# Kernel tuning notes

Hardware: AMD Instinct MI355X
Metric: run time of the kernel (lower is better)

## Reference

```python
import jax, jax.numpy as jnp
import numpy as np

N_NODES = 100000
N_EDGES = 1000000
N_RELS = 8
N_HEADS = 4
IN_FEAT = 64
OUT_FEAT = 64
D_HEAD = OUT_FEAT // N_HEADS
LEAKY_SLOPE = 0.2


def setup_inputs() -> dict:
    key = jax.random.key(0)
    ks = jax.random.split(key, 8)
    x = jax.random.normal(ks[0], (N_NODES, IN_FEAT), dtype=jnp.float32)
    src_idx = jax.random.randint(ks[1], (N_EDGES,), 0, N_NODES)
    dst_idx = jax.random.randint(ks[2], (N_EDGES,), 0, N_NODES)
    edge_rel = jnp.sort(jax.random.randint(ks[3], (N_EDGES,), 0, N_RELS))
    # xavier-ish small init for weights
    conv_weights = jax.random.normal(ks[4], (N_RELS, N_HEADS, IN_FEAT, D_HEAD), dtype=jnp.float32) * 0.1
    attn_l = jax.random.normal(ks[5], (N_RELS, N_HEADS, D_HEAD), dtype=jnp.float32) * 0.1
    attn_r = jax.random.normal(ks[6], (N_RELS, N_HEADS, D_HEAD), dtype=jnp.float32) * 0.1
    h_bias = jnp.zeros((OUT_FEAT,), dtype=jnp.float32)
    return {
        'x': x, 'src_idx': src_idx, 'dst_idx': dst_idx, 'edge_rel': edge_rel,
        'conv_weights': conv_weights, 'attn_l': attn_l, 'attn_r': attn_r,
        'h_bias': h_bias,
    }


def reference(x, src_idx, dst_idx, edge_rel, conv_weights, attn_l, attn_r, h_bias):
    N = x.shape[0]
    # Per-relation transform of all node features: [R, N, H, D]
    feat_all = jnp.einsum('ni,rhid->rnhd', x, conv_weights)
    # Per-relation attention logits per node: [R, N, H]
    el_all = jnp.einsum('rnhd,rhd->rnh', feat_all, attn_l)
    er_all = jnp.einsum('rnhd,rhd->rnh', feat_all, attn_r)
    # Gather per-edge quantities (relation-specific transform of src/dst)
    feat_e = feat_all[edge_rel, src_idx]          # [E, H, D]
    el = el_all[edge_rel, src_idx]                # [E, H]
    er = er_all[edge_rel, dst_idx]                # [E, H]
    s = jax.nn.leaky_relu(el + er, negative_slope=LEAKY_SLOPE)
    # Edge softmax over incoming edges of each destination node (per head)
    m = jax.ops.segment_max(s, dst_idx, num_segments=N)      # [N, H]
    e = jnp.exp(s - m[dst_idx])                               # [E, H]
    denom = jax.ops.segment_sum(e, dst_idx, num_segments=N)   # [N, H]
    w = e / jnp.maximum(denom[dst_idx], jnp.float32(1e-16))   # [E, H]
    # Weighted aggregation of source features into destination nodes
    agg = jax.ops.segment_sum(feat_e * w[..., None], dst_idx, num_segments=N)  # [N, H, D]
    h = agg.reshape(N, OUT_FEAT) + h_bias
    # activation=None, dropout in eval mode -> identity
    return h
```

## Files before the change

### kernel.cpp

```cpp
#include <hip/hip_runtime.h>
#include <hip/hip_bf16.h>

#define NN 100000
#define NE 1000000
#define NR 8

#define EB 1024
#define NBLK 977
#define NBUCK 196
#define NT (NBUCK*NBLK)
#define NBB 749

#define K3DPB 32
#define K3CAP 160

#define K0_BLKS  160
#define PRE_BLKS (K0_BLKS + NBLK)

typedef unsigned short u16;
typedef unsigned int u32;
typedef __attribute__((ext_vector_type(8))) short bf16x8;
typedef __attribute__((ext_vector_type(4))) float f32x4;

static __device__ __forceinline__ float bf2f(u16 u) {
    union { u32 i; float f; } v; v.i = ((u32)u) << 16; return v.f;
}
static __device__ __forceinline__ float bflo(u32 u) {
    union { u32 i; float f; } v; v.i = u << 16; return v.f;
}
static __device__ __forceinline__ float bfhi(u32 u) {
    union { u32 i; float f; } v; v.i = u & 0xffff0000u; return v.f;
}
static __device__ __forceinline__ u16 f2bf(float f) {
    __hip_bfloat16 h = __float2bfloat16(f);
    return *reinterpret_cast<u16*>(&h);
}
static __device__ __forceinline__ float ldf(const void* p, int idx, int isf32) {
    return isf32 ? ((const float*)p)[idx] : bf2f(((const u16*)p)[idx]);
}

static __device__ __forceinline__ int detect_wave(const u16* xw, int lane)
{
    int insane = 0;
    for (int k = lane; k < 512; k += 64) {
        u16 w = xw[k];
        int ex = (w >> 7) & 0xFF;
        bool sane = ((w & 0x7FFF) == 0) || (ex >= 96 && ex <= 159);
        insane += sane ? 0 : 1;
    }
    for (int off = 32; off; off >>= 1) insane += __shfl_down(insane, off);
    return insane;
}

__global__ __launch_bounds__(256) void k_pre(
    const void* __restrict__ xin, int* __restrict__ flag,
    const void* __restrict__ cw, const void* __restrict__ al,
    const void* __restrict__ ar, u16* __restrict__ Bpre,
    const int* __restrict__ dsti, int* __restrict__ histT)
{
    __shared__ int sflag;
    __shared__ int hist[NBUCK];
    int t = threadIdx.x;
    int b = blockIdx.x;

    if (b < K0_BLKS) {
        if (t < 64) {
            int insane = detect_wave((const u16*)xin, t);
            if (t == 0) {
                sflag = (insane > 50) ? 1 : 0;
                if (b == 0) *flag = sflag;
            }
        }
        __syncthreads();
        int isf32 = sflag;
        int tid = b * 256 + t;
        if (tid >= NR * 5120) return;
        int r = tid / 5120, rem = tid % 5120;
        int c = rem >> 3, j = rem & 7;
        int nt = c >> 7, kk = (c >> 6) & 1, lc = c & 63;
        int i = kk * 32 + ((lc >> 4) << 3) + j;
        int d = lc & 15;
        u16 val;
        if (nt < 4) {
            val = f2bf(ldf(cw, ((r * 4 + nt) * 64 + i) * 16 + d, isf32));
        } else if (d < 8) {
            int h = d >> 1;
            const void* attn = (d & 1) ? ar : al;
            float s = 0.f;
            for (int dd = 0; dd < 16; ++dd)
                s += ldf(cw, ((r * 4 + h) * 64 + i) * 16 + dd, isf32)
                   * ldf(attn, (r * 4 + h) * 16 + dd, isf32);
            val = f2bf(s);
        } else {
            val = 0;
        }
        Bpre[tid] = val;
    } else {
        int blk = b - K0_BLKS;
        if (t < NBUCK) hist[t] = 0;
        __syncthreads();
        int base = blk * EB;
        for (int j = 0; j < EB; j += 256) {
            int e = base + j + t;
            if (e < NE) atomicAdd(&hist[dsti[e] >> 9], 1);
        }
        __syncthreads();
        if (t < NBUCK) histT[t * NBLK + blk] = hist[t];
    }
}

__global__ __launch_bounds__(256) void k1_feat(
    const void* __restrict__ xin, const u16* __restrict__ Bpre,
    u16* __restrict__ feat_all, float* __restrict__ el_all, float* __restrict__ er_all)
{
    __shared__ u32 ldsT[2][64][32];
    int n0 = blockIdx.x * 64;
    int tid = threadIdx.x;
    int wave = tid >> 6, lane = tid & 63;
    int col = lane & 15, quad = lane >> 4;

    int insane = detect_wave((const u16*)xin, lane);
    insane = __shfl(insane, 0);
    int isf32 = (insane > 50) ? 1 : 0;

    int node = n0 + wave * 16 + col;
    int nclamp = node < NN ? node : NN - 1;
    bool nvalid = node < NN;

    bf16x8 afrag0, afrag1;
    if (!isf32) {
        const u16* xb = (const u16*)xin + nclamp * 64 + quad * 8;
        afrag0 = *(const bf16x8*)&xb[0];
        afrag1 = *(const bf16x8*)&xb[32];
    } else {
        const float* xf = (const float*)xin + nclamp * 64 + quad * 8;
#pragma unroll
        for (int j = 0; j < 8; ++j) {
            afrag0[j] = (short)f2bf(xf[j]);
            afrag1[j] = (short)f2bf(xf[32 + j]);
        }
    }

#pragma unroll 1
    for (int ch = 0; ch < 4; ++ch) {
#pragma unroll
        for (int rr = 0; rr < 2; ++rr) {
            int r = ch * 2 + rr;
            f32x4 acc[5];
#pragma unroll
            for (int nt = 0; nt < 5; ++nt) acc[nt] = f32x4{0.f, 0.f, 0.f, 0.f};
#pragma unroll
            for (int nt = 0; nt < 5; ++nt) {
                bf16x8 b0 = *(const bf16x8*)&Bpre[r * 5120 + ((nt * 2 + 0) * 64 + lane) * 8];
                bf16x8 b1 = *(const bf16x8*)&Bpre[r * 5120 + ((nt * 2 + 1) * 64 + lane) * 8];
                acc[nt] = __builtin_amdgcn_mfma_f32_16x16x32_bf16(b0, afrag0, acc[nt], 0, 0, 0);
                acc[nt] = __builtin_amdgcn_mfma_f32_16x16x32_bf16(b1, afrag1, acc[nt], 0, 0, 0);
            }

#pragma unroll
            for (int nt = 0; nt < 4; ++nt) {
                u32 lo = (u32)f2bf(acc[nt][0]) | ((u32)f2bf(acc[nt][1]) << 16);
                u32 hi = (u32)f2bf(acc[nt][2]) | ((u32)f2bf(acc[nt][3]) << 16);
                int w = (nt * 8 + quad * 2) ^ (col * 2);
                *(uint2*)&ldsT[rr][wave * 16 + col][w] = uint2{lo, hi};
            }
            if (nvalid && quad < 2) {
                int eb = (r * NN + node) * 4 + quad * 2;
                *(float2*)&el_all[eb] = float2{acc[4][0], acc[4][2]};
                *(float2*)&er_all[eb] = float2{acc[4][1], acc[4][3]};
            }
        }
        __syncthreads();

#pragma unroll
        for (int it = 0; it < 8; ++it) {
            int u = it * 256 + tid;
            int rr = u >> 10;
            int v = u & 1023;
            int nl = v >> 4;
            int p  = v & 15;
            int w  = (p * 2) ^ ((nl & 15) * 2);
            uint2 val = *(const uint2*)&ldsT[rr][nl][w];
            int nd = n0 + nl;
            if (nd < NN)
                *(uint2*)&feat_all[((ch * 2 + rr) * NN + nd) * 64 + p * 4] = val;
        }
        __syncthreads();
    }
}

__global__ __launch_bounds__(256) void k_scanB1(int* __restrict__ histT,
                                                int* __restrict__ bsum)
{
    __shared__ int wtot[4];
    int t = threadIdx.x;
    int gi = blockIdx.x * 256 + t;
    int v = (gi < NT) ? histT[gi] : 0;
    int lane = t & 63, w = t >> 6;
    int s = v;
#pragma unroll
    for (int m = 1; m < 64; m <<= 1) {
        int u = __shfl_up(s, m);
        if (lane >= m) s += u;
    }
    if (lane == 63) wtot[w] = s;
    __syncthreads();
    int wb = 0;
    for (int i = 0; i < w; ++i) wb += wtot[i];
    if (gi < NT) histT[gi] = wb + s - v;
    if (t == 255) bsum[blockIdx.x] = wb + s;
}

__global__ __launch_bounds__(1024) void k_scanB2(const int* __restrict__ bsum,
                                                 int* __restrict__ boff,
                                                 const int* __restrict__ histT,
                                                 int* __restrict__ bstart)
{
    __shared__ int wtot[16];
    __shared__ int sboff[NBB];
    int t = threadIdx.x;
    int v = (t < NBB) ? bsum[t] : 0;
    int lane = t & 63, w = t >> 6;
    int s = v;
#pragma unroll
    for (int m = 1; m < 64; m <<= 1) {
        int u = __shfl_up(s, m);
        if (lane >= m) s += u;
    }
    if (lane == 63) wtot[w] = s;
    __syncthreads();
    int wb = 0;
    for (int i = 0; i < w; ++i) wb += wtot[i];
    if (t < NBB) {
        int val = wb + s - v;
        boff[t] = val;
        sboff[t] = val;
    }
    __syncthreads();
    if (t < NBUCK) {
        int gi = t * NBLK;
        bstart[t] = histT[gi] + sboff[gi >> 8];
    }
    if (t == 0) bstart[NBUCK] = NE;
}

__global__ __launch_bounds__(256) void k_binC(
    const int* __restrict__ srci, const int* __restrict__ dsti,
    const int* __restrict__ reli, const int* __restrict__ histT,
    const int* __restrict__ boff, int* __restrict__ key_b)
{
    __shared__ int cur[NBUCK];
    int t = threadIdx.x, blk = blockIdx.x;
    if (t < NBUCK) {
        int gi = t * NBLK + blk;
        cur[t] = histT[gi] + boff[gi >> 8];
    }
    __syncthreads();
    int base = blk * EB;
    for (int j = 0; j < EB; j += 256) {
        int e = base + j + t;
        if (e < NE) {
            int d = dsti[e];
            int key = ((d & 511) << 20) | (reli[e] << 17) | srci[e];
            int pos = atomicAdd(&cur[d >> 9], 1);
            key_b[pos] = key;
        }
    }
}

__global__ __launch_bounds__(1024) void k_binD(
    const int* __restrict__ bstart, const int* __restrict__ key_b,
    int* __restrict__ key_s, int* __restrict__ off)
{
    __shared__ int cnt[512];
    __shared__ int wtot[8];
    int t = threadIdx.x, b = blockIdx.x;
    int s0 = bstart[b], s1 = bstart[b + 1];
    if (t < 512) cnt[t] = 0;
    __syncthreads();
    for (int j = s0 + t; j < s1; j += 1024)
        atomicAdd(&cnt[(key_b[j] >> 20) & 511], 1);
    __syncthreads();
    int excl = 0;
    if (t < 512) {
        int v = cnt[t];
        int lane = t & 63, w = t >> 6;
        int s = v;
#pragma unroll
        for (int m = 1; m < 64; m <<= 1) {
            int u = __shfl_up(s, m);
            if (lane >= m) s += u;
        }
        if (lane == 63) wtot[w] = s;
        __syncthreads();
        int wb = 0;
        for (int i = 0; i < w; ++i) wb += wtot[i];
        excl = s0 + wb + s - v;
        int d = (b << 9) + t;
        if (d < NN) off[d] = excl;
    } else {
        __syncthreads();
    }
    __syncthreads();
    if (t < 512) cnt[t] = excl;
    if (b == 0 && t == 0) off[NN] = NE;
    __syncthreads();
    for (int j = s0 + t; j < s1; j += 1024) {
        int key = key_b[j];
        int pos = atomicAdd(&cnt[(key >> 20) & 511], 1);
        key_s[pos] = key;
    }
}

__global__ __launch_bounds__(256) void k3_node(
    const int* __restrict__ off, const int* __restrict__ key_s,
    const float* __restrict__ el_all, const float* __restrict__ er_all,
    const u16* __restrict__ feat_all, const void* __restrict__ bias,
    const int* __restrict__ flag, void* __restrict__ out)
{
    __shared__ int   ldsOffs[K3DPB + 1];
    __shared__ int   ldsKey[4][K3CAP];
    __shared__ float ldsEE[4][K3CAP][4];
    int t = threadIdx.x;
    int wave = t >> 6, lane = t & 63;
    int dg = lane >> 3;
    int fl = lane & 7;
    int h  = fl >> 1;
    int d0 = blockIdx.x * K3DPB;
    int isf32 = *flag;

    if (t < K3DPB + 1) ldsOffs[t] = off[min(d0 + t, NN)];
    __syncthreads();

    int dlo = wave * 8;
    int estart = ldsOffs[dlo], eend = ldsOffs[dlo + 8];
    int scount = min(eend - estart, K3CAP);

    int dbase = d0 & ~511;
    for (int j = lane; j < scount; j += 64) {
        int key = key_s[estart + j];
        int rel = (key >> 17) & 7, src = key & 131071;
        int d = dbase | ((key >> 20) & 511);
        int kk = rel * NN + src;
        f32x4 el = *(const f32x4*)&el_all[kk * 4];
        f32x4 er = *(const f32x4*)&er_all[(rel * NN + d) * 4];
        f32x4 ee;
#pragma unroll
        for (int q = 0; q < 4; ++q) {
            float v = el[q] + er[q];
            v = v > 0.f ? v : 0.2f * v;
            ee[q] = __expf(v);
        }
        ldsKey[wave][j] = kk;
        *(f32x4*)&ldsEE[wave][j][0] = ee;
    }

    float bv[8];
#pragma unroll
    for (int q = 0; q < 8; ++q) bv[q] = ldf(bias, fl * 8 + q, isf32);

    int nl = dlo + dg;
    int d = d0 + nl;
    int s  = ldsOffs[nl] - estart;
    int e1 = ldsOffs[nl + 1] - estart;
    float acc[8] = {0.f, 0.f, 0.f, 0.f, 0.f, 0.f, 0.f, 0.f};
    float accW = 0.f;

    int e1c = min(e1, K3CAP);
    for (int base = s; base < e1c; base += 4) {
        int kk[4]; float w[4];
#pragma unroll
        for (int q = 0; q < 4; ++q) {
            int idx = base + q;
            bool vld = idx < e1c;
            kk[q] = vld ? ldsKey[wave][idx] : ldsKey[wave][base];
            w[q]  = vld ? ldsEE[wave][idx][h] : 0.f;
        }
        uint4 u[4];
#pragma unroll
        for (int q = 0; q < 4; ++q)
            u[q] = *(const uint4*)&feat_all[kk[q] * 64 + fl * 8];
#pragma unroll
        for (int q = 0; q < 4; ++q) {
            acc[0] += bflo(u[q].x) * w[q];
            acc[1] += bfhi(u[q].x) * w[q];
            acc[2] += bflo(u[q].y) * w[q];
            acc[3] += bfhi(u[q].y) * w[q];
            acc[4] += bflo(u[q].z) * w[q];
            acc[5] += bfhi(u[q].z) * w[q];
            acc[6] += bflo(u[q].w) * w[q];
            acc[7] += bfhi(u[q].w) * w[q];
            accW += w[q];
        }
    }
    for (int j = max(s, K3CAP); j < e1; ++j) {
        int key = key_s[estart + j];
        int rel = (key >> 17) & 7, src = key & 131071;
        int kk0 = rel * NN + src;
        float v = el_all[kk0 * 4 + h] + er_all[(rel * NN + d) * 4 + h];
        v = v > 0.f ? v : 0.2f * v;
        float w0 = __expf(v);
        uint4 u = *(const uint4*)&feat_all[kk0 * 64 + fl * 8];
        acc[0] += bflo(u.x) * w0;
        acc[1] += bfhi(u.x) * w0;
        acc[2] += bflo(u.y) * w0;
        acc[3] += bfhi(u.y) * w0;
        acc[4] += bflo(u.z) * w0;
        acc[5] += bfhi(u.z) * w0;
        acc[6] += bflo(u.w) * w0;
        acc[7] += bfhi(u.w) * w0;
        accW += w0;
    }

    {
        float invh = 1.f / fmaxf(accW, 1e-16f);
        float o[8];
#pragma unroll
        for (int q = 0; q < 8; ++q) o[q] = acc[q] * invh + bv[q];
        if (isf32) {
            ((f32x4*)out)[d * 16 + fl * 2]     = f32x4{o[0], o[1], o[2], o[3]};
            ((f32x4*)out)[d * 16 + fl * 2 + 1] = f32x4{o[4], o[5], o[6], o[7]};
        } else {
            uint4 st;
            st.x = (u32)f2bf(o[0]) | ((u32)f2bf(o[1]) << 16);
            st.y = (u32)f2bf(o[2]) | ((u32)f2bf(o[3]) << 16);
            st.z = (u32)f2bf(o[4]) | ((u32)f2bf(o[5]) << 16);
            st.w = (u32)f2bf(o[6]) | ((u32)f2bf(o[7]) << 16);
            *(uint4*)&((u16*)out)[d * 64 + fl * 8] = st;
        }
    }
}

extern "C" void kernel_launch(void* const* d_in, const int* in_sizes, int n_in,
                              void* d_out, int out_size, void* d_ws, size_t ws_size,
                              hipStream_t stream)
{
    const void* x   = d_in[0];
    const int* srci = (const int*)d_in[1];
    const int* dsti = (const int*)d_in[2];
    const int* reli = (const int*)d_in[3];
    const void* cw  = d_in[4];
    const void* al  = d_in[5];
    const void* ar  = d_in[6];
    const void* hb  = d_in[7];

    char* ws = (char*)d_ws;
    u16*   feat_all = (u16*)  (ws + 0);
    float* el_all   = (float*)(ws + 102400000);
    float* er_all   = (float*)(ws + 115200000);
    int*   key_s    = (int*)  (ws + 128000000);
    int*   key_b    = (int*)  (ws + 132000000);
    int*   off      = (int*)  (ws + 136000000);
    int*   histT    = (int*)  (ws + 136400064);
    int*   bsum     = (int*)  (ws + 137166032);
    int*   boff     = (int*)  (ws + 137169040);
    int*   bstart   = (int*)  (ws + 137172048);
    u16*   Bpre     = (u16*)  (ws + 137172880);
    int*   flag     = (int*)  (ws + 137254800);

    k_pre<<<PRE_BLKS, 256, 0, stream>>>(x, flag, cw, al, ar, Bpre, dsti, histT);
    k1_feat<<<(NN + 63) / 64, 256, 0, stream>>>(x, Bpre, feat_all, el_all, er_all);
    k_scanB1<<<NBB, 256, 0, stream>>>(histT, bsum);
    k_scanB2<<<1, 1024, 0, stream>>>(bsum, boff, histT, bstart);
    k_binC<<<NBLK, 256, 0, stream>>>(srci, dsti, reli, histT, boff, key_b);
    k_binD<<<NBUCK, 1024, 0, stream>>>(bstart, key_b, key_s, off);
    k3_node<<<(NN + 31) / 32, 256, 0, stream>>>(off, key_s, el_all, er_all, feat_all,
                                                hb, flag, d_out);
}
```

Baseline: 201.6 us.

## Interleave feature transform blocks with sort stages in fused launches

Splits the dense per-relation feature transform (k1) into four chunks and co-launches each chunk alongside one stage of the destination-sort pipeline (scan1, scan2, binning, per-bucket sort) in a single fused kernel with a shared LDS buffer. The latency-bound sort stages, especially the single-block scan, now run concurrently with compute-heavy MFMA blocks instead of serially. scanB2 and binD are rewritten to use 256 threads with carried multi-pass scans, so the fused kernel has a uniform block size. The tradeoff is a larger shared-memory footprint for every block, which can lower occupancy, plus more branching and uneven work across blocks.

```diff
diff --git a/kernel.cpp b/kernel.cpp
--- a/kernel.cpp
+++ b/kernel.cpp
@@ -16,6 +16,12 @@
 
 #define K0_BLKS  160
 #define PRE_BLKS (K0_BLKS + NBLK)
+
+#define K1CH 1563
+#define F1K 390
+#define F2K 390
+#define F3K 391
+#define F4K 392
 
 typedef unsigned short u16;
 typedef unsigned int u32;
@@ -109,12 +115,13 @@
     }
 }
 
-__global__ __launch_bounds__(256) void k1_feat(
+static __device__ __forceinline__ void k1_body(
+    int cb, unsigned char* smem,
     const void* __restrict__ xin, const u16* __restrict__ Bpre,
     u16* __restrict__ feat_all, float* __restrict__ el_all, float* __restrict__ er_all)
 {
-    __shared__ u32 ldsT[2][64][32];
-    int n0 = blockIdx.x * 64;
+    u32 (*ldsT)[64][32] = (u32 (*)[64][32])smem;
+    int n0 = cb * 64;
     int tid = threadIdx.x;
     int wave = tid >> 6, lane = tid & 63;
     int col = lane & 15, quad = lane >> 4;
@@ -156,7 +163,6 @@
                 acc[nt] = __builtin_amdgcn_mfma_f32_16x16x32_bf16(b0, afrag0, acc[nt], 0, 0, 0);
                 acc[nt] = __builtin_amdgcn_mfma_f32_16x16x32_bf16(b1, afrag1, acc[nt], 0, 0, 0);
             }
-
 #pragma unroll
             for (int nt = 0; nt < 4; ++nt) {
                 u32 lo = (u32)f2bf(acc[nt][0]) | ((u32)f2bf(acc[nt][1]) << 16);
@@ -171,7 +177,6 @@
             }
         }
         __syncthreads();
-
 #pragma unroll
         for (int it = 0; it < 8; ++it) {
             int u = it * 256 + tid;
@@ -189,12 +194,12 @@
     }
 }
 
-__global__ __launch_bounds__(256) void k_scanB1(int* __restrict__ histT,
-                                                int* __restrict__ bsum)
-{
-    __shared__ int wtot[4];
+static __device__ __forceinline__ void scanB1_body(
+    int b, unsigned char* smem, int* __restrict__ histT, int* __restrict__ bsum)
+{
+    int* wtot = (int*)smem;
     int t = threadIdx.x;
-    int gi = blockIdx.x * 256 + t;
+    int gi = b * 256 + t;
     int v = (gi < NT) ? histT[gi] : 0;
     int lane = t & 63, w = t >> 6;
     int s = v;
@@ -208,35 +213,40 @@
     int wb = 0;
     for (int i = 0; i < w; ++i) wb += wtot[i];
     if (gi < NT) histT[gi] = wb + s - v;
-    if (t == 255) bsum[blockIdx.x] = wb + s;
-}
-
-__global__ __launch_bounds__(1024) void k_scanB2(const int* __restrict__ bsum,
-                                                 int* __restrict__ boff,
-                                                 const int* __restrict__ histT,
-                                                 int* __restrict__ bstart)
-{
-    __shared__ int wtot[16];
-    __shared__ int sboff[NBB];
+    if (t == 255) bsum[b] = wb + s;
+}
+
+static __device__ __forceinline__ void scanB2_body(
+    unsigned char* smem, const int* __restrict__ bsum, int* __restrict__ boff,
+    const int* __restrict__ histT, int* __restrict__ bstart)
+{
+    int* wtot  = (int*)smem;
+    int* sboff = (int*)(smem + 16);
+    int* carry = (int*)(smem + 16 + 4 * NBB);
     int t = threadIdx.x;
-    int v = (t < NBB) ? bsum[t] : 0;
-    int lane = t & 63, w = t >> 6;
-    int s = v;
-#pragma unroll
-    for (int m = 1; m < 64; m <<= 1) {
-        int u = __shfl_up(s, m);
-        if (lane >= m) s += u;
-    }
-    if (lane == 63) wtot[w] = s;
-    __syncthreads();
-    int wb = 0;
-    for (int i = 0; i < w; ++i) wb += wtot[i];
-    if (t < NBB) {
-        int val = wb + s - v;
-        boff[t] = val;
-        sboff[t] = val;
-    }
-    __syncthreads();
+    if (t == 0) *carry = 0;
+    __syncthreads();
+    for (int c = 0; c < 3; ++c) {
+        int idx = c * 256 + t;
+        int v = (idx < NBB) ? bsum[idx] : 0;
+        int lane = t & 63, w = t >> 6;
+        int s = v;
+#pragma unroll
+        for (int m = 1; m < 64; m <<= 1) {
+            int u = __shfl_up(s, m);
+            if (lane >= m) s += u;
+        }
+        if (lane == 63) wtot[w] = s;
+        __syncthreads();
+        int wb = 0;
+        for (int i = 0; i < w; ++i) wb += wtot[i];
+        int ex = *carry + wb + s - v;
+        if (idx < NBB) sboff[idx] = ex;
+        __syncthreads();
+        if (t == 255) *carry += wb + s;
+        __syncthreads();
+    }
+    for (int i = t; i < NBB; i += 256) boff[i] = sboff[i];
     if (t < NBUCK) {
         int gi = t * NBLK;
         bstart[t] = histT[gi] + sboff[gi >> 8];
@@ -244,19 +254,20 @@
     if (t == 0) bstart[NBUCK] = NE;
 }
 
-__global__ __launch_bounds__(256) void k_binC(
+static __device__ __forceinline__ void binC_body(
+    int b, unsigned char* smem,
     const int* __restrict__ srci, const int* __restrict__ dsti,
     const int* __restrict__ reli, const int* __restrict__ histT,
     const int* __restrict__ boff, int* __restrict__ key_b)
 {
-    __shared__ int cur[NBUCK];
-    int t = threadIdx.x, blk = blockIdx.x;
+    int* cur = (int*)smem;
+    int t = threadIdx.x;
     if (t < NBUCK) {
-        int gi = t * NBLK + blk;
+        int gi = t * NBLK + b;
         cur[t] = histT[gi] + boff[gi >> 8];
     }
     __syncthreads();
-    int base = blk * EB;
+    int base = b * EB;
     for (int j = 0; j < EB; j += 256) {
         int e = base + j + t;
         if (e < NE) {
@@ -268,22 +279,26 @@
     }
 }
 
-__global__ __launch_bounds__(1024) void k_binD(
+static __device__ __forceinline__ void binD_body(
+    int b, unsigned char* smem,
     const int* __restrict__ bstart, const int* __restrict__ key_b,
     int* __restrict__ key_s, int* __restrict__ off)
 {
-    __shared__ int cnt[512];
-    __shared__ int wtot[8];
-    int t = threadIdx.x, b = blockIdx.x;
+    int* cnt   = (int*)smem;
+    int* wtot  = (int*)(smem + 2048);
+    int* carry = (int*)(smem + 2064);
+    int t = threadIdx.x;
     int s0 = bstart[b], s1 = bstart[b + 1];
-    if (t < 512) cnt[t] = 0;
-    __syncthreads();
-    for (int j = s0 + t; j < s1; j += 1024)
+    cnt[t] = 0; cnt[t + 256] = 0;
+    if (t == 0) *carry = 0;
+    __syncthreads();
+    for (int j = s0 + t; j < s1; j += 256)
         atomicAdd(&cnt[(key_b[j] >> 20) & 511], 1);
     __syncthreads();
-    int excl = 0;
-    if (t < 512) {
-        int v = cnt[t];
+    int excl[2];
+#pragma unroll
+    for (int c = 0; c < 2; ++c) {
+        int v = cnt[c * 256 + t];
         int lane = t & 63, w = t >> 6;
         int s = v;
 #pragma unroll
@@ -295,21 +310,46 @@
         __syncthreads();
         int wb = 0;
         for (int i = 0; i < w; ++i) wb += wtot[i];
-        excl = s0 + wb + s - v;
-        int d = (b << 9) + t;
-        if (d < NN) off[d] = excl;
-    } else {
-        __syncthreads();
-    }
-    __syncthreads();
-    if (t < 512) cnt[t] = excl;
+        excl[c] = s0 + *carry + wb + s - v;
+        __syncthreads();
+        if (t == 255) *carry += wb + s;
+        __syncthreads();
+    }
+#pragma unroll
+    for (int c = 0; c < 2; ++c) {
+        int d = (b << 9) + c * 256 + t;
+        if (d < NN) off[d] = excl[c];
+    }
+    cnt[t] = excl[0]; cnt[t + 256] = excl[1];
     if (b == 0 && t == 0) off[NN] = NE;
     __syncthreads();
-    for (int j = s0 + t; j < s1; j += 1024) {
+    for (int j = s0 + t; j < s1; j += 256) {
         int key = key_b[j];
         int pos = atomicAdd(&cnt[(key >> 20) & 511], 1);
         key_s[pos] = key;
     }
+}
+
+__global__ __launch_bounds__(256) void k_fused(
+    int stage, int nsort, int k1base,
+    const void* __restrict__ xin, const u16* __restrict__ Bpre,
+    u16* __restrict__ feat_all, float* __restrict__ el_all, float* __restrict__ er_all,
+    const int* __restrict__ srci, const int* __restrict__ dsti,
+    const int* __restrict__ reli,
+    int* __restrict__ histT, int* __restrict__ bsum, int* __restrict__ boff,
+    int* __restrict__ bstart, int* __restrict__ key_b, int* __restrict__ key_s,
+    int* __restrict__ off)
+{
+    __shared__ alignas(16) unsigned char smem[16448];
+    int b = blockIdx.x;
+    if (b >= nsort) {
+        k1_body(k1base + (b - nsort), smem, xin, Bpre, feat_all, el_all, er_all);
+        return;
+    }
+    if (stage == 0)      scanB1_body(b, smem, histT, bsum);
+    else if (stage == 1) scanB2_body(smem, bsum, boff, histT, bstart);
+    else if (stage == 2) binC_body(b, smem, srci, dsti, reli, histT, boff, key_b);
+    else                 binD_body(b, smem, bstart, key_b, key_s, off);
 }
 
 __global__ __launch_bounds__(256) void k3_node(
@@ -459,11 +499,20 @@
     int*   flag     = (int*)  (ws + 137254800);
 
     k_pre<<<PRE_BLKS, 256, 0, stream>>>(x, flag, cw, al, ar, Bpre, dsti, histT);
-    k1_feat<<<(NN + 63) / 64, 256, 0, stream>>>(x, Bpre, feat_all, el_all, er_all);
-    k_scanB1<<<NBB, 256, 0, stream>>>(histT, bsum);
-    k_scanB2<<<1, 1024, 0, stream>>>(bsum, boff, histT, bstart);
-    k_binC<<<NBLK, 256, 0, stream>>>(srci, dsti, reli, histT, boff, key_b);
-    k_binD<<<NBUCK, 1024, 0, stream>>>(bstart, key_b, key_s, off);
+
+    k_fused<<<NBB + F1K, 256, 0, stream>>>(0, NBB, 0,
+        x, Bpre, feat_all, el_all, er_all, srci, dsti, reli,
+        histT, bsum, boff, bstart, key_b, key_s, off);
+    k_fused<<<1 + F2K, 256, 0, stream>>>(1, 1, F1K,
+        x, Bpre, feat_all, el_all, er_all, srci, dsti, reli,
+        histT, bsum, boff, bstart, key_b, key_s, off);
+    k_fused<<<NBLK + F3K, 256, 0, stream>>>(2, NBLK, F1K + F2K,
+        x, Bpre, feat_all, el_all, er_all, srci, dsti, reli,
+        histT, bsum, boff, bstart, key_b, key_s, off);
+    k_fused<<<NBUCK + F4K, 256, 0, stream>>>(3, NBUCK, F1K + F2K + F3K,
+        x, Bpre, feat_all, el_all, er_all, srci, dsti, reli,
+        histT, bsum, boff, bstart, key_b, key_s, off);
+
     k3_node<<<(NN + 31) / 32, 256, 0, stream>>>(off, key_s, el_all, er_all, feat_all,
                                                 hb, flag, d_out);
 }
```

New measurement: 216.4 us. 7.4% more time.
